# Kernel tuning notes

Hardware: AMD Instinct MI355X
Metric: run time of the kernel (lower is better)

Reference implementation:

```python
import jax, jax.numpy as jnp
import numpy as np

IN_DIM = 16
HID = 384            # hidden_dim
POS_DIM = HID // 2   # 192, ContinuousSincosEmbed dim
NDIM = 3
G = 32 * 32 * 32     # num_grid_points = prod(resolution)
N_MESH = 50000
E = 131072


def _linear_params(key, fan_in, fan_out):
    kw, kb = jax.random.split(key)
    bound = 1.0 / np.sqrt(fan_in)
    w = jax.random.uniform(kw, (fan_in, fan_out), jnp.float32, -bound, bound)
    b = jax.random.uniform(kb, (fan_out,), jnp.float32, -bound, bound)
    return w, b


def setup_inputs() -> dict:
    key = jax.random.key(0)
    ks = jax.random.split(key, 12)
    inp = {}
    inp["x"] = jax.random.normal(ks[0], (N_MESH, IN_DIM), jnp.float32)
    inp["mesh_pos"] = jax.random.uniform(ks[1], (N_MESH, NDIM), jnp.float32) * 32.0
    inp["grid_pos"] = jax.random.uniform(ks[2], (G, NDIM), jnp.float32) * 32.0
    # edges: column 0 = grid_idx (sorted, as required by segment_csr), column 1 = mesh_idx
    grid_idx = jnp.sort(jax.random.randint(ks[3], (E,), 0, G, jnp.int64))
    mesh_idx = jax.random.randint(ks[4], (E,), 0, N_MESH, jnp.int64)
    inp["mesh_to_grid_edges"] = jnp.stack([grid_idx, mesh_idx], axis=1)
    # input_proj: Linear(16,384) GELU Linear(384,384) GELU Linear(384,384)
    inp["w_in1"], inp["b_in1"] = _linear_params(ks[5], IN_DIM, HID)
    inp["w_in2"], inp["b_in2"] = _linear_params(ks[6], HID, HID)
    inp["w_in3"], inp["b_in3"] = _linear_params(ks[7], HID, HID)
    # message: Linear(768,768) GELU Linear(768,768) GELU Linear(768,384)
    inp["w_m1"], inp["b_m1"] = _linear_params(ks[8], 2 * HID, 2 * HID)
    inp["w_m2"], inp["b_m2"] = _linear_params(ks[9], 2 * HID, 2 * HID)
    inp["w_m3"], inp["b_m3"] = _linear_params(ks[10], 2 * HID, HID)
    return inp


def _sincos_embed(coords):
    # ContinuousSincosEmbed(dim=192, ndim=3): 64 channels per coord, no padding
    eff = POS_DIM // NDIM  # 64
    omega = 1.0 / (10000.0 ** (jnp.arange(0, eff, 2, dtype=jnp.float32) / eff))  # [32]
    out = coords[:, :, None] * omega  # [N, 3, 32]
    emb = jnp.concatenate([jnp.sin(out), jnp.cos(out)], axis=-1)  # [N, 3, 64]
    return emb.reshape(coords.shape[0], POS_DIM)  # [N, 192]


def reference(x, mesh_pos, grid_pos, mesh_to_grid_edges,
              w_in1, b_in1, w_in2, b_in2, w_in3, b_in3,
              w_m1, b_m1, w_m2, b_m2, w_m3, b_m3):
    gelu = lambda v: jax.nn.gelu(v, approximate=False)
    # input projection on mesh features
    h = gelu(x @ w_in1 + b_in1)
    h = gelu(h @ w_in2 + b_in2)
    h = h @ w_in3 + b_in3                                  # [N_mesh, 384]
    mesh_feat = jnp.concatenate([h, _sincos_embed(mesh_pos)], axis=1)  # [N_mesh, 576]
    grid_emb = _sincos_embed(grid_pos)                     # [G, 192]
    grid_idx = mesh_to_grid_edges[:, 0]
    mesh_idx = mesh_to_grid_edges[:, 1]
    # gather + concat -> [E, 768]
    e = jnp.concatenate([mesh_feat[mesh_idx], grid_emb[grid_idx]], axis=1)
    m = gelu(e @ w_m1 + b_m1)
    m = gelu(m @ w_m2 + b_m2)
    m = m @ w_m3 + b_m3                                    # [E, 384]
    # segment mean over grid points (empty segments -> 0, like segment_csr)
    num_grid = grid_pos.shape[0]
    sums = jax.ops.segment_sum(m, grid_idx, num_segments=num_grid)
    cnt = jax.ops.segment_sum(jnp.ones((m.shape[0],), m.dtype), grid_idx, num_segments=num_grid)
    out = sums / jnp.maximum(cnt, 1.0)[:, None]            # [G, 384]
    return out.reshape(-1, G, HID)                         # [batch, num_grid_points, dim]
```

## Files before the change

### kernel.cpp

```cpp
#include <hip/hip_runtime.h>
#include <hip/hip_bf16.h>

#define NMESH 50000
#define GRIDN 32768
#define NEDGE 131072
#define HID 384

using f32x4 = __attribute__((ext_vector_type(4))) float;
using bfrag = __attribute__((ext_vector_type(8))) short;
using i32x4 = __attribute__((ext_vector_type(4))) int;

__device__ __forceinline__ float gelu_f(float v) {
    return 0.5f * v * (1.0f + erff(v * 0.70710678118654752f));
}

__device__ __forceinline__ void load_lds16(const void* g, void* l) {
    __builtin_amdgcn_global_load_lds(
        (const __attribute__((address_space(1))) void*)g,
        (__attribute__((address_space(3))) void*)l,
        16, 0, 0);
}

__device__ __forceinline__ void xcd_swizzle(int& bx, int& by) {
    int gx = gridDim.x;
    int nwg = gx * gridDim.y;
    int l = blockIdx.y * gx + blockIdx.x;
    int q = nwg >> 3, r = nwg & 7;
    int xcd = l & 7, pos = l >> 3;
    int nl = (xcd < r ? xcd * (q + 1) : r * (q + 1) + (xcd - r) * q) + pos;
    by = nl / gx;
    bx = nl - by * gx;
}

__device__ __forceinline__ bfrag fuse8(i32x4 u, i32x4 v) {
    bfrag ub = *reinterpret_cast<bfrag*>(&u);
    bfrag vb = *reinterpret_cast<bfrag*>(&v);
    bfrag o;
    #pragma unroll
    for (int i = 0; i < 8; i++) {
        unsigned short us = (unsigned short)ub[i], vs = (unsigned short)vb[i];
        float a = __bfloat162float(*(__hip_bfloat16*)&us) + __bfloat162float(*(__hip_bfloat16*)&vs);
        a = gelu_f(a);
        __hip_bfloat16 hb = __float2bfloat16(a);
        o[i] = *(short*)&hb;
    }
    return o;
}

__global__ void transpose_to_bf16(const float* __restrict__ w, __hip_bfloat16* __restrict__ wt,
                                  int K, int N, int k0) {
    int idx = blockIdx.x * blockDim.x + threadIdx.x;
    if (idx >= K * N) return;
    int n = idx / K;
    int k = idx - n * K;
    wt[idx] = __float2bfloat16(w[(size_t)(k0 + k) * N + n]);
}

__global__ void fold_w3_wm1(const float* __restrict__ w3, const float* __restrict__ wm1,
                            __hip_bfloat16* __restrict__ wtf) {
    int idx = blockIdx.x * blockDim.x + threadIdx.x;
    if (idx >= 576 * 768) return;
    int k = idx / 768;
    int n = idx - k * 768;
    float acc;
    if (k < 384) {
        acc = 0.f;
        #pragma unroll 4
        for (int j = 0; j < 384; j++)
            acc = fmaf(w3[k * 384 + j], wm1[j * 768 + n], acc);
    } else {
        acc = wm1[(size_t)k * 768 + n];
    }
    wtf[(size_t)n * 576 + k] = __float2bfloat16(acc);
}

__global__ void fold_bias(const float* __restrict__ b3, const float* __restrict__ wm1,
                          const float* __restrict__ bm1, float* __restrict__ bf) {
    int n = blockIdx.x * blockDim.x + threadIdx.x;
    if (n >= 768) return;
    float acc = bm1[n];
    #pragma unroll 4
    for (int k = 0; k < 384; k++) acc = fmaf(b3[k], wm1[(size_t)k * 768 + n], acc);
    bf[n] = acc;
}

__global__ void calc_rowstart(const int* __restrict__ edges, int* __restrict__ rs) {
    int g = blockIdx.x * blockDim.x + threadIdx.x;
    if (g > GRIDN) return;
    int l = 0, r = NEDGE;
    while (l < r) { int m = (l + r) >> 1; if (edges[2 * m] < g) l = m + 1; else r = m; }
    rs[g] = l;
}

__global__ void embed_kernel(const float* __restrict__ pos, __hip_bfloat16* __restrict__ outp,
                             int n, int stride, int coloff) {
    int idx = blockIdx.x * blockDim.x + threadIdx.x;
    if (idx >= n * 96) return;
    int nn = idx / 96;
    int rr = idx - nn * 96;
    int d = rr >> 5;
    int k = rr & 31;
    float v = pos[nn * 3 + d];
    float omega = expf(-0.28782313662425575f * (float)k);
    float a = v * omega;
    __hip_bfloat16* o = outp + (size_t)nn * stride + coloff + d * 64 + k;
    o[0]  = __float2bfloat16(sinf(a));
    o[32] = __float2bfloat16(cosf(a));
}

__global__ void lin1_kernel(const float* __restrict__ x, const float* __restrict__ w,
                            const float* __restrict__ b, __hip_bfloat16* __restrict__ h1) {
    int idx = blockIdx.x * blockDim.x + threadIdx.x;
    if (idx >= NMESH * HID) return;
    int m = idx / HID;
    int n = idx - m * HID;
    float acc = b[n];
    const float* xr = x + m * 16;
    #pragma unroll
    for (int k = 0; k < 16; k++) acc = fmaf(xr[k], w[k * HID + n], acc);
    h1[idx] = __float2bfloat16(gelu_f(acc));
}

template<bool GELU, bool F32OUT, bool SEGA>
__launch_bounds__(256, 3)
__global__ void mfma_gemm(const __hip_bfloat16* __restrict__ A,
                          const __hip_bfloat16* __restrict__ Wt,
                          const float* __restrict__ bias,
                          void* __restrict__ Cv, void* __restrict__ Cv2,
                          int M, int N, int K, int ldc,
                          const int* __restrict__ seg_edges, int seg_e0) {
    __shared__ __align__(16) __hip_bfloat16 As[3][4096];
    __shared__ __align__(16) __hip_bfloat16 Bs[3][4096];

    const int t = threadIdx.x;
    const int lane = t & 63;
    const int wave = t >> 6;
    const int wm0 = (wave >> 1) * 64;
    const int wn0 = (wave & 1) * 64;

    int bx, by;
    xcd_swizzle(bx, by);
    const int row0 = by * 128;
    const int col0 = bx * 128;

    const int rS0 = t >> 2;
    const int rS1 = rS0 + 64;
    const int kcS = (t & 3) ^ ((t >> 3) & 3);

    const __hip_bfloat16* aP0 = A + (size_t)min(row0 + rS0, M - 1) * K;
    const __hip_bfloat16* aP1 = A + (size_t)min(row0 + rS1, M - 1) * K;
    const __hip_bfloat16* bP0 = Wt + (size_t)(col0 + rS0) * K;
    const __hip_bfloat16* bP1 = Wt + (size_t)(col0 + rS1) * K;

    const int off0 = (wave * 64) * 16;
    const int off1 = (256 + wave * 64) * 16;

    f32x4 acc[4][4] = {};

    const int kq = lane >> 4;
    const int lr = lane & 15;
    const int kqx = kq ^ ((lr >> 1) & 3);
    const int rdA = (wm0 + lr) * 32 + kqx * 8;
    const int rdB = (wn0 + lr) * 32 + kqx * 8;

    const int nsteps = K >> 5;

    auto stage = [&](int ks, int buf) {
        int k = ks * 32 + kcS * 8;
        load_lds16(aP0 + k, (char*)As[buf] + off0);
        load_lds16(aP1 + k, (char*)As[buf] + off1);
        load_lds16(bP0 + k, (char*)Bs[buf] + off0);
        load_lds16(bP1 + k, (char*)Bs[buf] + off1);
    };

    stage(0, 0);
    stage(1, 1);

    int cur = 0;
    int stg = 2;
    for (int ks = 0; ks < nsteps; ks++) {
        if (ks + 1 < nsteps) {
            asm volatile("s_waitcnt vmcnt(4)" ::: "memory");
        } else {
            asm volatile("s_waitcnt vmcnt(0)" ::: "memory");
        }
        __builtin_amdgcn_s_barrier();
        if (ks + 2 < nsteps) stage(ks + 2, stg);

        bfrag aF[4], bF[4];
        #pragma unroll
        for (int i = 0; i < 4; i++) {
            aF[i] = *reinterpret_cast<const bfrag*>(&As[cur][rdA + i * 512]);
            bF[i] = *reinterpret_cast<const bfrag*>(&Bs[cur][rdB + i * 512]);
        }
        asm volatile("s_waitcnt lgkmcnt(0)" ::: "memory");
        __builtin_amdgcn_sched_barrier(0);
        __builtin_amdgcn_s_setprio(1);
        #pragma unroll
        for (int i = 0; i < 4; i++) {
            #pragma unroll
            for (int j = 0; j < 4; j++) {
                acc[i][j] = __builtin_amdgcn_mfma_f32_16x16x32_bf16(aF[i], bF[j], acc[i][j], 0, 0, 0);
            }
        }
        __builtin_amdgcn_s_setprio(0);

        cur = (cur == 2) ? 0 : cur + 1;
        stg = (stg == 2) ? 0 : stg + 1;
    }

    if constexpr (SEGA) {
        float* o0 = (float*)Cv;
        float* o1 = (float*)Cv2;
        #pragma unroll
        for (int i = 0; i < 4; i++) {
            int rbase = seg_e0 + row0 + wm0 + i * 16 + kq * 4;
            int g0 = seg_edges[2 * (rbase + 0)];
            int g1 = seg_edges[2 * (rbase + 1)];
            int g2 = seg_edges[2 * (rbase + 2)];
            int g3 = seg_edges[2 * (rbase + 3)];
            bool same = (g0 == g1) & (g1 == g2) & (g2 == g3);
            #pragma unroll
            for (int j = 0; j < 4; j++) {
                int col = col0 + wn0 + j * 16 + lr;
                float* base = (col < 384) ? (o0 + col) : (o1 + (col - 384));
                float v0 = gelu_f(acc[i][j][0] + bias[col]);
                float v1 = gelu_f(acc[i][j][1] + bias[col]);
                float v2 = gelu_f(acc[i][j][2] + bias[col]);
                float v3 = gelu_f(acc[i][j][3] + bias[col]);
                if (same) {
                    unsafeAtomicAdd(base + (size_t)g0 * 384, v0 + v1 + v2 + v3);
                } else {
                    unsafeAtomicAdd(base + (size_t)g0 * 384, v0);
                    unsafeAtomicAdd(base + (size_t)g1 * 384, v1);
                    unsafeAtomicAdd(base + (size_t)g2 * 384, v2);
                    unsafeAtomicAdd(base + (size_t)g3 * 384, v3);
                }
            }
        }
    } else {
        #pragma unroll
        for (int i = 0; i < 4; i++) {
            #pragma unroll
            for (int j = 0; j < 4; j++) {
                #pragma unroll
                for (int r = 0; r < 4; r++) {
                    int row = row0 + wm0 + i * 16 + kq * 4 + r;
                    int col = col0 + wn0 + j * 16 + lr;
                    if (row < M) {
                        float v = acc[i][j][r] + bias[col];
                        if constexpr (GELU) v = gelu_f(v);
                        if constexpr (F32OUT)
                            ((float*)Cv)[(size_t)row * ldc + col] = v;
                        else
                            ((__hip_bfloat16*)Cv)[(size_t)row * ldc + col] = __float2bfloat16(v);
                    }
                }
            }
        }
    }
}

__global__ void fuse_m1(const __hip_bfloat16* __restrict__ U, const __hip_bfloat16* __restrict__ V,
                        const int* __restrict__ edges, int e0, int ne,
                        __hip_bfloat16* __restrict__ m1c) {
    int idx = blockIdx.x * blockDim.x + threadIdx.x;
    if (idx >= ne * 96) return;
    int e = idx / 96;
    int c8 = (idx - e * 96) * 8;
    int ge = e0 + e;
    int mi = edges[2 * ge + 1];
    int gi = edges[2 * ge + 0];
    i32x4 u = *reinterpret_cast<const i32x4*>(U + (size_t)mi * 768 + c8);
    i32x4 v = *reinterpret_cast<const i32x4*>(V + (size_t)gi * 768 + c8);
    *reinterpret_cast<bfrag*>(m1c + (size_t)e * 768 + c8) = fuse8(u, v);
}

__global__ void mean_bf16(const float* __restrict__ s0, const float* __restrict__ s1,
                          const int* __restrict__ rs, __hip_bfloat16* __restrict__ mm) {
    int idx = blockIdx.x * blockDim.x + threadIdx.x;
    int base = idx * 4;
    if (base >= GRIDN * 768) return;
    int g = base / 768;
    int c = base - g * 768;
    int cnt = rs[g + 1] - rs[g];
    float inv = 1.0f / (float)max(cnt, 1);
    float4 v = (c < 384) ? *reinterpret_cast<const float4*>(s0 + (size_t)g * 384 + c)
                         : *reinterpret_cast<const float4*>(s1 + (size_t)g * 384 + (c - 384));
    __hip_bfloat16 o[4] = {__float2bfloat16(v.x * inv), __float2bfloat16(v.y * inv),
                           __float2bfloat16(v.z * inv), __float2bfloat16(v.w * inv)};
    *reinterpret_cast<uint2*>(mm + base) = *reinterpret_cast<const uint2*>(o);
}

__global__ void fix_empty(const int* __restrict__ rs, float* __restrict__ out) {
    int g = blockIdx.x * blockDim.x + threadIdx.x;
    if (g >= GRIDN || (rs[g + 1] - rs[g]) != 0) return;
    float* row = out + (size_t)g * HID;
    for (int c = 0; c < HID; c++) row[c] = 0.f;
}

__global__ void seg_partial(const int* __restrict__ edges, int e0, int e1,
                            const __hip_bfloat16* __restrict__ m3c, float* __restrict__ out) {
    int g = blockIdx.x;
    int l = e0, r = e1;
    while (l < r) { int mid = (l + r) >> 1; if (edges[2 * mid] < g) l = mid + 1; else r = mid; }
    int lo = l;
    r = e1;
    while (l < r) { int mid = (l + r) >> 1; if (edges[2 * mid] <= g) l = mid + 1; else r = mid; }
    int hi = l;
    if (lo >= hi) return;
    int c = threadIdx.x;
    float s0 = 0.f, s1 = 0.f, s2 = 0.f;
    for (int e = lo; e < hi; e++) {
        const __hip_bfloat16* rp = m3c + (size_t)(e - e0) * HID;
        s0 += __bfloat162float(rp[c]);
        s1 += __bfloat162float(rp[c + 128]);
        s2 += __bfloat162float(rp[c + 256]);
    }
    float* orow = out + (size_t)g * HID;
    orow[c] += s0;
    orow[c + 128] += s1;
    orow[c + 256] += s2;
}

__global__ void seg_div(const int* __restrict__ edges, float* __restrict__ out) {
    int g = blockIdx.x;
    int l = 0, r = NEDGE;
    while (l < r) { int mid = (l + r) >> 1; if (edges[2 * mid] < g) l = mid + 1; else r = mid; }
    int lo = l;
    r = NEDGE;
    while (l < r) { int mid = (l + r) >> 1; if (edges[2 * mid] <= g) l = mid + 1; else r = mid; }
    int cnt = l - lo;
    float inv = 1.0f / (float)max(cnt, 1);
    int c = threadIdx.x;
    float* orow = out + (size_t)g * HID;
    orow[c] *= inv;
    orow[c + 128] *= inv;
    orow[c + 256] *= inv;
}

extern "C" void kernel_launch(void* const* d_in, const int* in_sizes, int n_in,
                              void* d_out, int out_size, void* d_ws, size_t ws_size,
                              hipStream_t stream) {
    const float* x        = (const float*)d_in[0];
    const float* mesh_pos = (const float*)d_in[1];
    const float* grid_pos = (const float*)d_in[2];
    const int*   edges    = (const int*)d_in[3];
    const float* w1  = (const float*)d_in[4];
    const float* b1  = (const float*)d_in[5];
    const float* w2  = (const float*)d_in[6];
    const float* b2  = (const float*)d_in[7];
    const float* w3  = (const float*)d_in[8];
    const float* b3  = (const float*)d_in[9];
    const float* wm1 = (const float*)d_in[10];
    const float* bm1 = (const float*)d_in[11];
    const float* wm2 = (const float*)d_in[12];
    const float* bm2 = (const float*)d_in[13];
    const float* wm3 = (const float*)d_in[14];
    const float* bm3 = (const float*)d_in[15];
    float* out = (float*)d_out;

    auto rnd = [](size_t b) { return (b + 255) & ~(size_t)255; };
    const size_t wbytes = rnd((size_t)384 * 384 * 2) + rnd((size_t)768 * 576 * 2) +
                          rnd((size_t)768 * 192 * 2) + rnd((size_t)768 * 768 * 2) +
                          rnd((size_t)384 * 768 * 2) + rnd(768 * 4) * 2 +
                          rnd((size_t)(GRIDN + 1) * 4);
    const size_t szU    = rnd((size_t)NMESH * 768 * 2);
    const size_t szV    = rnd((size_t)GRIDN * 768 * 2);
    const size_t szMesh = rnd((size_t)NMESH * 576 * 2);
    const size_t szS2   = rnd((size_t)GRIDN * 384 * 4);
    const size_t szM1   = rnd((size_t)32768 * 768 * 2);

    const size_t NEED_FOLD = wbytes + szU + szV + szS2 + szM1;

    char* p = (char*)d_ws;
    auto alloc = [&](size_t b) { char* r = p; p += (b + 255) & ~(size_t)255; return r; };

    __hip_bfloat16* wt2   = (__hip_bfloat16*)alloc((size_t)384 * 384 * 2);
    __hip_bfloat16* wtm1f = (__hip_bfloat16*)alloc((size_t)768 * 576 * 2);
    __hip_bfloat16* wtm1v = (__hip_bfloat16*)alloc((size_t)768 * 192 * 2);
    __hip_bfloat16* wtm2  = (__hip_bfloat16*)alloc((size_t)768 * 768 * 2);
    __hip_bfloat16* wtm3  = (__hip_bfloat16*)alloc((size_t)384 * 768 * 2);
    float* zeros          = (float*)alloc(768 * 4);
    float* bf             = (float*)alloc(768 * 4);
    int* rs               = (int*)alloc((size_t)(GRIDN + 1) * 4);
    char* Ur              = alloc(szU);
    char* Vr              = alloc(szV);

    __hip_bfloat16* U  = (__hip_bfloat16*)Ur;
    __hip_bfloat16* V  = (__hip_bfloat16*)Vr;
    __hip_bfloat16* h1 = (__hip_bfloat16*)Ur;

    hipMemsetAsync(zeros, 0, 768 * 4, stream);

    transpose_to_bf16<<<(384 * 384 + 255) / 256, 256, 0, stream>>>(w2, wt2, 384, 384, 0);
    transpose_to_bf16<<<(768 * 192 + 255) / 256, 256, 0, stream>>>(wm1, wtm1v, 192, 768, 576);
    transpose_to_bf16<<<(768 * 768 + 255) / 256, 256, 0, stream>>>(wm2, wtm2, 768, 768, 0);
    transpose_to_bf16<<<(768 * 384 + 255) / 256, 256, 0, stream>>>(wm3, wtm3, 768, 384, 0);
    fold_w3_wm1<<<(576 * 768 + 255) / 256, 256, 0, stream>>>(w3, wm1, wtm1f);
    fold_bias<<<3, 256, 0, stream>>>(b3, wm1, bm1, bf);
    calc_rowstart<<<(GRIDN + 1 + 255) / 256, 256, 0, stream>>>(edges, rs);

    if (ws_size >= NEED_FOLD) {
        const int CH = 32768;
        const int NCH = NEDGE / CH;
        char* S2r = alloc(szS2);
        char* CA  = alloc(szM1);

        float* S2             = (float*)S2r;
        __hip_bfloat16* meshf2 = (__hip_bfloat16*)S2r;
        __hip_bfloat16* gridf  = (__hip_bfloat16*)(S2r + szMesh);
        __hip_bfloat16* m1c    = (__hip_bfloat16*)CA;
        __hip_bfloat16* meanM2 = (__hip_bfloat16*)CA;

        embed_kernel<<<(NMESH * 96 + 255) / 256, 256, 0, stream>>>(mesh_pos, meshf2, NMESH, 576, 384);
        embed_kernel<<<(GRIDN * 96 + 255) / 256, 256, 0, stream>>>(grid_pos, gridf, GRIDN, 192, 0);

        lin1_kernel<<<(NMESH * HID + 255) / 256, 256, 0, stream>>>(x, w1, b1, h1);

        mfma_gemm<true, false, false><<<dim3(3, 391), 256, 0, stream>>>(
            h1, wt2, b2, meshf2, nullptr, NMESH, 384, 384, 576, nullptr, 0);
        mfma_gemm<false, false, false><<<dim3(6, 391), 256, 0, stream>>>(
            meshf2, wtm1f, bf, U, nullptr, NMESH, 768, 576, 768, nullptr, 0);
        mfma_gemm<false, false, false><<<dim3(6, 256), 256, 0, stream>>>(
            gridf, wtm1v, zeros, V, nullptr, GRIDN, 768, 192, 768, nullptr, 0);

        hipMemsetAsync(out, 0, (size_t)GRIDN * 384 * 4, stream);
        hipMemsetAsync(S2, 0, (size_t)GRIDN * 384 * 4, stream);

        for (int c = 0; c < NCH; c++) {
            int e0 = c * CH;
            fuse_m1<<<(CH * 96 + 255) / 256, 256, 0, stream>>>(U, V, edges, e0, CH, m1c);
            mfma_gemm<true, false, true><<<dim3(6, CH / 128), 256, 0, stream>>>(
                m1c, wtm2, bm2, out, S2, CH, 768, 768, 768, edges, e0);
        }

        mean_bf16<<<(GRIDN * 768 / 4 + 255) / 256, 256, 0, stream>>>(out, S2, rs, meanM2);
        mfma_gemm<false, true, false><<<dim3(3, 256), 256, 0, stream>>>(
            meanM2, wtm3, bm3, out, nullptr, GRIDN, 384, 768, 384, nullptr, 0);
        fix_empty<<<(GRIDN + 255) / 256, 256, 0, stream>>>(rs, out);
    } else {
        const int CH = 32768;
        const int NCH = NEDGE / CH;
        char* CA = alloc(2 * rnd((size_t)CH * 768 * 2));

        __hip_bfloat16* meshf2 = (__hip_bfloat16*)CA;
        __hip_bfloat16* gridf  = (__hip_bfloat16*)(CA + szMesh);
        __hip_bfloat16* m1c    = (__hip_bfloat16*)CA;
        __hip_bfloat16* m2c    = (__hip_bfloat16*)(CA + rnd((size_t)CH * 768 * 2));
        __hip_bfloat16* m3c    = m1c;

        hipMemsetAsync(out, 0, (size_t)GRIDN * HID * 4, stream);

        embed_kernel<<<(NMESH * 96 + 255) / 256, 256, 0, stream>>>(mesh_pos, meshf2, NMESH, 576, 384);
        embed_kernel<<<(GRIDN * 96 + 255) / 256, 256, 0, stream>>>(grid_pos, gridf, GRIDN, 192, 0);

        lin1_kernel<<<(NMESH * HID + 255) / 256, 256, 0, stream>>>(x, w1, b1, h1);

        mfma_gemm<true, false, false><<<dim3(3, 391), 256, 0, stream>>>(
            h1, wt2, b2, meshf2, nullptr, NMESH, 384, 384, 576, nullptr, 0);
        mfma_gemm<false, false, false><<<dim3(6, 391), 256, 0, stream>>>(
            meshf2, wtm1f, bf, U, nullptr, NMESH, 768, 576, 768, nullptr, 0);
        mfma_gemm<false, false, false><<<dim3(6, 256), 256, 0, stream>>>(
            gridf, wtm1v, zeros, V, nullptr, GRIDN, 768, 192, 768, nullptr, 0);

        for (int c = 0; c < NCH; c++) {
            int e0 = c * CH;
            fuse_m1<<<(CH * 96 + 255) / 256, 256, 0, stream>>>(U, V, edges, e0, CH, m1c);
            mfma_gemm<true, false, false><<<dim3(6, CH / 128), 256, 0, stream>>>(
                m1c, wtm2, bm2, m2c, nullptr, CH, 768, 768, 768, nullptr, 0);
            mfma_gemm<false, false, false><<<dim3(3, CH / 128), 256, 0, stream>>>(
                m2c, wtm3, bm3, m3c, nullptr, CH, 384, 768, 384, nullptr, 0);
            seg_partial<<<GRIDN, 128, 0, stream>>>(edges, e0, e0 + CH, m3c, out);
        }

        seg_div<<<GRIDN, 128, 0, stream>>>(edges, out);
    }
}
```

Before: 1.006 ms.

## Fuse edge gather and m1 GELU combine into the m2 GEMM A-tile load

Result: slower. 1.078 ms (+7.1%).

```diff
diff --git a/kernel.cpp b/kernel.cpp
--- a/kernel.cpp
+++ b/kernel.cpp
@@ -261,6 +261,134 @@
     }
 }
 
+__launch_bounds__(256, 3)
+__global__ void mfma_gemm_m2s(const __hip_bfloat16* __restrict__ U,
+                              const __hip_bfloat16* __restrict__ V,
+                              const int* __restrict__ edges, int e0,
+                              const __hip_bfloat16* __restrict__ Wt,
+                              const float* __restrict__ bias,
+                              float* __restrict__ o0, float* __restrict__ o1) {
+    const int K = 768;
+    __shared__ __align__(16) __hip_bfloat16 As[2][4096];
+    __shared__ __align__(16) __hip_bfloat16 Bs[2][4096];
+
+    const int t = threadIdx.x;
+    const int lane = t & 63;
+    const int wave = t >> 6;
+    const int wm0 = (wave >> 1) * 64;
+    const int wn0 = (wave & 1) * 64;
+
+    int bx, by;
+    xcd_swizzle(bx, by);
+    const int row0 = by * 128;
+    const int col0 = bx * 128;
+
+    const int kcA = t & 3;
+    const int rS0 = t >> 2;
+    const int rS1 = rS0 + 64;
+    const int er0 = e0 + row0 + rS0;
+    const int er1 = e0 + row0 + rS1;
+    const __hip_bfloat16* uP0 = U + (size_t)edges[2 * er0 + 1] * 768;
+    const __hip_bfloat16* vP0 = V + (size_t)edges[2 * er0 + 0] * 768;
+    const __hip_bfloat16* uP1 = U + (size_t)edges[2 * er1 + 1] * 768;
+    const __hip_bfloat16* vP1 = V + (size_t)edges[2 * er1 + 0] * 768;
+    const int dA0 = kcA * 1024 + ((rS0 ^ (kcA << 1)) << 3);
+    const int dA1 = kcA * 1024 + ((rS1 ^ (kcA << 1)) << 3);
+
+    const int kcB = (t & 3) ^ ((t >> 3) & 3);
+    const __hip_bfloat16* bP0 = Wt + (size_t)(col0 + rS0) * K;
+    const __hip_bfloat16* bP1 = Wt + (size_t)(col0 + rS1) * K;
+    const int offB0 = (wave * 64) * 16;
+    const int offB1 = (256 + wave * 64) * 16;
+
+    f32x4 acc[4][4] = {};
+
+    const int kq = lane >> 4;
+    const int lr = lane & 15;
+    const int rdA = kq * 1024 + ((lr ^ (kq << 1)) << 3) + wm0 * 8;
+    const int kqx = kq ^ ((lr >> 1) & 3);
+    const int rdB = (wn0 + lr) * 32 + kqx * 8;
+
+    const int nsteps = K >> 5;
+
+    {
+        int k = kcA * 8;
+        i32x4 u0 = *reinterpret_cast<const i32x4*>(uP0 + k);
+        i32x4 v0 = *reinterpret_cast<const i32x4*>(vP0 + k);
+        i32x4 u1 = *reinterpret_cast<const i32x4*>(uP1 + k);
+        i32x4 v1 = *reinterpret_cast<const i32x4*>(vP1 + k);
+        *reinterpret_cast<bfrag*>(&As[0][dA0]) = fuse8(u0, v0);
+        *reinterpret_cast<bfrag*>(&As[0][dA1]) = fuse8(u1, v1);
+        int kb = kcB * 8;
+        load_lds16(bP0 + kb, (char*)Bs[0] + offB0);
+        load_lds16(bP1 + kb, (char*)Bs[0] + offB1);
+    }
+    __syncthreads();
+
+    int cur = 0;
+    for (int ks = 0; ks < nsteps; ks++) {
+        const bool more = (ks + 1 < nsteps);
+        i32x4 u0, v0, u1, v1;
+        if (more) {
+            int k = (ks + 1) * 32 + kcA * 8;
+            u0 = *reinterpret_cast<const i32x4*>(uP0 + k);
+            v0 = *reinterpret_cast<const i32x4*>(vP0 + k);
+            u1 = *reinterpret_cast<const i32x4*>(uP1 + k);
+            v1 = *reinterpret_cast<const i32x4*>(vP1 + k);
+            int kb = (ks + 1) * 32 + kcB * 8;
+            load_lds16(bP0 + kb, (char*)Bs[cur ^ 1] + offB0);
+            load_lds16(bP1 + kb, (char*)Bs[cur ^ 1] + offB1);
+        }
+
+        bfrag aF[4], bF[4];
+        #pragma unroll
+        for (int i = 0; i < 4; i++) {
+            aF[i] = *reinterpret_cast<const bfrag*>(&As[cur][rdA + i * 128]);
+            bF[i] = *reinterpret_cast<const bfrag*>(&Bs[cur][rdB + i * 512]);
+        }
+        #pragma unroll
+        for (int i = 0; i < 4; i++) {
+            #pragma unroll
+            for (int j = 0; j < 4; j++) {
+                acc[i][j] = __builtin_amdgcn_mfma_f32_16x16x32_bf16(aF[i], bF[j], acc[i][j], 0, 0, 0);
+            }
+        }
+        if (more) {
+            *reinterpret_cast<bfrag*>(&As[cur ^ 1][dA0]) = fuse8(u0, v0);
+            *reinterpret_cast<bfrag*>(&As[cur ^ 1][dA1]) = fuse8(u1, v1);
+        }
+        __syncthreads();
+        cur ^= 1;
+    }
+
+    #pragma unroll
+    for (int i = 0; i < 4; i++) {
+        int rbase = e0 + row0 + wm0 + i * 16 + kq * 4;
+        int g0 = edges[2 * (rbase + 0)];
+        int g1 = edges[2 * (rbase + 1)];
+        int g2 = edges[2 * (rbase + 2)];
+        int g3 = edges[2 * (rbase + 3)];
+        bool same = (g0 == g1) & (g1 == g2) & (g2 == g3);
+        #pragma unroll
+        for (int j = 0; j < 4; j++) {
+            int col = col0 + wn0 + j * 16 + lr;
+            float* base = (col < 384) ? (o0 + col) : (o1 + (col - 384));
+            float v0 = gelu_f(acc[i][j][0] + bias[col]);
+            float v1 = gelu_f(acc[i][j][1] + bias[col]);
+            float v2 = gelu_f(acc[i][j][2] + bias[col]);
+            float v3 = gelu_f(acc[i][j][3] + bias[col]);
+            if (same) {
+                unsafeAtomicAdd(base + (size_t)g0 * 384, v0 + v1 + v2 + v3);
+            } else {
+                unsafeAtomicAdd(base + (size_t)g0 * 384, v0);
+                unsafeAtomicAdd(base + (size_t)g1 * 384, v1);
+                unsafeAtomicAdd(base + (size_t)g2 * 384, v2);
+                unsafeAtomicAdd(base + (size_t)g3 * 384, v3);
+            }
+        }
+    }
+}
+
 __global__ void fuse_m1(const __hip_bfloat16* __restrict__ U, const __hip_bfloat16* __restrict__ V,
                         const int* __restrict__ edges, int e0, int ne,
                         __hip_bfloat16* __restrict__ m1c) {
@@ -410,7 +538,6 @@
         float* S2             = (float*)S2r;
         __hip_bfloat16* meshf2 = (__hip_bfloat16*)S2r;
         __hip_bfloat16* gridf  = (__hip_bfloat16*)(S2r + szMesh);
-        __hip_bfloat16* m1c    = (__hip_bfloat16*)CA;
         __hip_bfloat16* meanM2 = (__hip_bfloat16*)CA;
 
         embed_kernel<<<(NMESH * 96 + 255) / 256, 256, 0, stream>>>(mesh_pos, meshf2, NMESH, 576, 384);
@@ -430,9 +557,8 @@
 
         for (int c = 0; c < NCH; c++) {
             int e0 = c * CH;
-            fuse_m1<<<(CH * 96 + 255) / 256, 256, 0, stream>>>(U, V, edges, e0, CH, m1c);
-            mfma_gemm<true, false, true><<<dim3(6, CH / 128), 256, 0, stream>>>(
-                m1c, wtm2, bm2, out, S2, CH, 768, 768, 768, edges, e0);
+            mfma_gemm_m2s<<<dim3(6, CH / 128), 256, 0, stream>>>(
+                U, V, edges, e0, wtm2, bm2, out, S2);
         }
 
         mean_bf16<<<(GRIDN * 768 / 4 + 255) / 256, 256, 0, stream>>>(out, S2, rs, meanM2);
```
